# Performance work log

Hardware: AMD Instinct MI355X
Metric: run time of the kernel (lower is better)

Reference implementation:

```python
import jax, jax.numpy as jnp
import numpy as np

L = 10
DIM = 4
TABLE = 1 << 16
BASE_RES = 16.0
PLS = 2.0
HID = 64
SCALE_MULTI = 0.5
DENSITY_OFFSET = -1.0
SCENE_SCALING = 2.0
PRIMES = (np.uint32(1), np.uint32(2654435761), np.uint32(805459861))


def _safe_exp(x):
    return jnp.exp(jnp.clip(x, -30.0, 10.0))


def _l2norm(x, eps=1e-8):
    return x / jnp.sqrt(jnp.sum(x * x, -1, keepdims=True) + eps)


def _circumcenters(tets):
    # tets: [T,4,3]; solve 2(vi-v0).c = |vi|^2-|v0|^2
    v0 = tets[:, 0]
    A = 2.0 * (tets[:, 1:] - v0[:, None, :]) + 1e-6 * jnp.eye(3, dtype=tets.dtype)
    b = jnp.sum(tets[:, 1:] ** 2, -1) - jnp.sum(v0 ** 2, -1)[:, None]
    c = jnp.linalg.solve(A, b[..., None])[..., 0]
    r = jnp.linalg.norm(c - v0, axis=-1)
    return c, r


def _project_to_tet(p, tets):
    # clamp-and-renormalize barycentric coordinates (approximate projection)
    v0 = tets[:, 0]
    E = tets[:, 1:] - v0[:, None, :]
    M = jnp.einsum('tid,tjd->tij', E, E) + 1e-6 * jnp.eye(3, dtype=tets.dtype)
    rhs = jnp.einsum('tid,td->ti', E, p - v0)
    lam = jnp.linalg.solve(M, rhs[..., None])[..., 0]
    bary = jnp.concatenate([1.0 - lam.sum(-1, keepdims=True), lam], -1)
    bary = jnp.clip(bary, 0.0, 1.0)
    bary = bary / jnp.clip(bary.sum(-1, keepdims=True), 1e-6, None)
    return jnp.einsum('tv,tvd->td', bary, tets)


def _contract_mean_std(x, std):
    # mipnerf-360 style scene contraction of mean; std scaled by |J| ~ 1/n^2
    n = jnp.maximum(jnp.linalg.norm(x, axis=-1, keepdims=True), 1e-9)
    cx = jnp.where(n <= 1.0, x, (2.0 - 1.0 / n) * x / n)
    cs = std * jnp.where(n[..., 0] <= 1.0, 1.0, 1.0 / (n[..., 0] ** 2))
    return cx, cs


def _hash_encode(pos, tables):
    # pos [T,3] in [0,1); tables [L, TABLE, DIM]; multiresolution hash grid
    mask = np.uint32(TABLE - 1)
    pos = jnp.clip(pos, 0.0, 1.0 - 1e-6)
    feats = []
    for l in range(L):
        res = float(np.floor(BASE_RES * (PLS ** l)))
        x = pos * res
        f = jnp.floor(x)
        w = x - f
        fi = f.astype(jnp.uint32)
        acc = jnp.zeros(pos.shape[:-1] + (DIM,), pos.dtype)
        for cz in (0, 1):
            for cy in (0, 1):
                for cx in (0, 1):
                    c = fi + jnp.asarray((cx, cy, cz), jnp.uint32)
                    h = ((c[..., 0] * PRIMES[0]) ^ (c[..., 1] * PRIMES[1]) ^ (c[..., 2] * PRIMES[2])) & mask
                    wt = ((w[..., 0] if cx else 1.0 - w[..., 0]) *
                          (w[..., 1] if cy else 1.0 - w[..., 1]) *
                          (w[..., 2] if cz else 1.0 - w[..., 2]))
                    acc = acc + tables[l][h.astype(jnp.int32)] * wt[..., None]
        feats.append(acc)
    return jnp.stack(feats, axis=1)  # [T, L, DIM]


def _forward(vertices, indices, center, tables, W1, b1, W2, b2, W3, b3):
    tets = vertices[indices]  # [T,4,3] gather
    cc, radius = _circumcenters(tets)
    cc = _project_to_tet(cc, tets)
    normalized = (cc - center) / SCENE_SCALING
    cv, cr = _contract_mean_std(normalized, radius / SCENE_SCALING)
    cr = cr * SCALE_MULTI
    n = jnp.arange(L, dtype=vertices.dtype)
    erf_x = 1.0 / jnp.sqrt(PLS * 4.0 * n[None, :] * cr[:, None] + 1e-12)
    scaling = jax.lax.erf(erf_x)  # [T, L] per-level erf anti-aliasing scale
    pos = cv * 0.25 + 0.5  # contracted [-2,2] -> [0,1]
    feats = _hash_encode(pos, tables) * scaling[..., None]
    h = feats.reshape(feats.shape[0], L * DIM)
    h = jax.nn.selu(h @ W1 + b1)
    h = jax.nn.selu(h @ W2 + b2)
    out = h @ W3 + b3  # [T, 13]
    density = _safe_exp(out[:, 0] + DENSITY_OFFSET)
    pairs = ((0, 1), (0, 2), (0, 3), (1, 2), (1, 3), (2, 3))
    el = jnp.stack([jnp.linalg.norm(tets[:, i] - tets[:, j], axis=1) for i, j in pairs], 0).max(0)
    alpha = 1.0 - jnp.exp(-density * el)
    V = vertices.shape[0]
    vertex_alpha = jnp.zeros((V,), vertices.dtype).at[indices].max(
        jnp.broadcast_to(alpha[:, None], indices.shape))  # scatter amax
    fs = out[:, 1:]
    base = fs[:, :3] + 0.5
    grads = jnp.clip(base[:, :, None], 0.0, None) * jnp.tanh(fs[:, 3:12].reshape(-1, 3, 3))
    offs = _l2norm(tets - cc[:, None, :])
    vcol = base[:, None, :] + jnp.einsum('tcd,tvd->tvc', grads, offs)  # [T,4,3]
    return vertex_alpha, vcol


def setup_inputs() -> dict:
    key = jax.random.key(0)
    ks = jax.random.split(key, 8)
    V, T = 100000, 500000
    vertices = jax.random.normal(ks[0], (V, 3), jnp.float32) * 0.5
    indices = jax.random.randint(ks[1], (T, 4), 0, V, jnp.int32)
    center = jnp.zeros((1, 3), jnp.float32)
    tables = jax.random.normal(ks[2], (L, TABLE, DIM), jnp.float32) * 1e-2
    def lin(k, i, o):
        s = (6.0 / (i + o)) ** 0.5
        return jax.random.uniform(k, (i, o), jnp.float32, -s, s)
    return dict(vertices=vertices, indices=indices, center=center, tables=tables,
                W1=lin(ks[3], L * DIM, HID), b1=jnp.zeros((HID,), jnp.float32),
                W2=lin(ks[4], HID, HID), b2=jnp.zeros((HID,), jnp.float32),
                W3=lin(ks[5], HID, 13), b3=jnp.zeros((13,), jnp.float32))


def reference(vertices, indices, center, tables, W1, b1, W2, b2, W3, b3):
    return _forward(vertices, indices, center, tables, W1, b1, W2, b2, W3, b3)
```

## Files before the change

### kernel.cpp

```cpp
#include <hip/hip_runtime.h>
#include <math.h>

#define NLVL 10
#define TBL 65536
#define NHID 64
#define NIN 40
#define LDP 68

typedef __attribute__((ext_vector_type(8))) short bf16x8;
typedef __attribute__((ext_vector_type(4))) float f32x4;

__device__ __forceinline__ float selu_f(float x) {
    return 1.0507009873554805f * (x > 0.0f ? x : 1.6732632423543772f * (__expf(x) - 1.0f));
}
__device__ __forceinline__ float fast_tanh(float x) {
    float xx = fminf(fmaxf(x, -15.0f), 15.0f);
    float t = __expf(2.0f * xx);
    return (t - 1.0f) / (t + 1.0f);
}
__device__ __forceinline__ unsigned short f2bf(float x) {
    unsigned u = __float_as_uint(x);
    unsigned r = (u + 0x7FFFu + ((u >> 16) & 1u)) >> 16;
    return (unsigned short)r;
}
__device__ __forceinline__ float bf2f(unsigned short h) {
    return __uint_as_float(((unsigned)h) << 16);
}
__device__ __forceinline__ short2 split_bf(float x) {
    unsigned short h = f2bf(x);
    float r = x - bf2f(h);
    short2 s;
    s.x = (short)h;
    s.y = (short)f2bf(r);
    return s;
}

__device__ __forceinline__ void solve3d(const double A[3][3], const double b[3], double x[3]) {
    double a00=A[0][0], a01=A[0][1], a02=A[0][2];
    double a10=A[1][0], a11=A[1][1], a12=A[1][2];
    double a20=A[2][0], a21=A[2][1], a22=A[2][2];
    double C00 =  (a11*a22 - a12*a21);
    double C01 = -(a10*a22 - a12*a20);
    double C02 =  (a10*a21 - a11*a20);
    double C10 = -(a01*a22 - a02*a21);
    double C11 =  (a00*a22 - a02*a20);
    double C12 = -(a00*a21 - a01*a20);
    double C20 =  (a01*a12 - a02*a11);
    double C21 = -(a00*a12 - a02*a10);
    double C22 =  (a00*a11 - a01*a10);
    double det = a00*C00 + a01*C01 + a02*C02;
    double inv = 1.0 / det;
    x[0] = (C00*b[0] + C10*b[1] + C20*b[2]) * inv;
    x[1] = (C01*b[0] + C11*b[1] + C21*b[2]) * inv;
    x[2] = (C02*b[0] + C12*b[1] + C22*b[2]) * inv;
}

__global__ void __launch_bounds__(256) zero_alpha_kernel(float* out, int V) {
    int i = blockIdx.x * blockDim.x + threadIdx.x;
    if (i < V) out[i] = 0.0f;
}

__global__ void __launch_bounds__(256) geom_kernel(
    const float* __restrict__ vertices,
    const int*   __restrict__ indices,
    const float* __restrict__ center,
    float* __restrict__ aux, int T)
{
    int t = blockIdx.x * blockDim.x + threadIdx.x;
    if (t >= T) return;

    double p[4][3];
    #pragma unroll
    for (int v = 0; v < 4; ++v) {
        int vid = indices[t*4+v];
        p[v][0] = (double)vertices[vid*3+0];
        p[v][1] = (double)vertices[vid*3+1];
        p[v][2] = (double)vertices[vid*3+2];
    }

    double A[3][3], bb[3];
    double v0sq = p[0][0]*p[0][0] + p[0][1]*p[0][1] + p[0][2]*p[0][2];
    #pragma unroll
    for (int i = 0; i < 3; ++i) {
        #pragma unroll
        for (int j = 0; j < 3; ++j)
            A[i][j] = 2.0*(p[i+1][j] - p[0][j]) + (i==j ? 1e-6 : 0.0);
        bb[i] = p[i+1][0]*p[i+1][0] + p[i+1][1]*p[i+1][1] + p[i+1][2]*p[i+1][2] - v0sq;
    }
    double c[3];
    solve3d(A, bb, c);
    double dx0 = c[0]-p[0][0], dy0 = c[1]-p[0][1], dz0 = c[2]-p[0][2];
    double radius = sqrt(dx0*dx0 + dy0*dy0 + dz0*dz0);

    double E[3][3];
    #pragma unroll
    for (int i = 0; i < 3; ++i)
        #pragma unroll
        for (int j = 0; j < 3; ++j)
            E[i][j] = p[i+1][j] - p[0][j];
    double M[3][3], rhs[3];
    #pragma unroll
    for (int i = 0; i < 3; ++i) {
        #pragma unroll
        for (int k = 0; k < 3; ++k)
            M[i][k] = E[i][0]*E[k][0] + E[i][1]*E[k][1] + E[i][2]*E[k][2] + (i==k ? 1e-6 : 0.0);
        rhs[i] = E[i][0]*dx0 + E[i][1]*dy0 + E[i][2]*dz0;
    }
    double lam[3];
    solve3d(M, rhs, lam);
    double bary[4];
    bary[0] = 1.0 - lam[0] - lam[1] - lam[2];
    bary[1] = lam[0]; bary[2] = lam[1]; bary[3] = lam[2];
    double bs = 0.0;
    #pragma unroll
    for (int v = 0; v < 4; ++v) {
        bary[v] = fmin(fmax(bary[v], 0.0), 1.0);
        bs += bary[v];
    }
    bs = fmax(bs, 1e-6);
    double cc[3];
    #pragma unroll
    for (int j = 0; j < 3; ++j)
        cc[j] = (bary[0]*p[0][j] + bary[1]*p[1][j] + bary[2]*p[2][j] + bary[3]*p[3][j]) / bs;

    double xv[3];
    xv[0] = (cc[0] - (double)center[0]) * 0.5;
    xv[1] = (cc[1] - (double)center[1]) * 0.5;
    xv[2] = (cc[2] - (double)center[2]) * 0.5;
    double nrm = sqrt(xv[0]*xv[0] + xv[1]*xv[1] + xv[2]*xv[2]);
    double n = fmax(nrm, 1e-9);
    double cv[3], cs;
    if (n <= 1.0) {
        cv[0]=xv[0]; cv[1]=xv[1]; cv[2]=xv[2];
        cs = radius * 0.5;
    } else {
        double f = (2.0 - 1.0/n) / n;
        cv[0]=xv[0]*f; cv[1]=xv[1]*f; cv[2]=xv[2]*f;
        cs = radius * 0.5 / (n*n);
    }
    float crf = (float)(cs * 0.5);

    float pos0 = fminf(fmaxf((float)(cv[0]*0.25 + 0.5), 0.0f), 1.0f - 1e-6f);
    float pos1 = fminf(fmaxf((float)(cv[1]*0.25 + 0.5), 0.0f), 1.0f - 1e-6f);
    float pos2 = fminf(fmaxf((float)(cv[2]*0.25 + 0.5), 0.0f), 1.0f - 1e-6f);

    float el = 0.0f;
    #pragma unroll
    for (int a = 0; a < 3; ++a)
        #pragma unroll
        for (int bq = a+1; bq < 4; ++bq) {
            float ddx = (float)(p[a][0]-p[bq][0]);
            float ddy = (float)(p[a][1]-p[bq][1]);
            float ddz = (float)(p[a][2]-p[bq][2]);
            el = fmaxf(el, sqrtf(ddx*ddx + ddy*ddy + ddz*ddz));
        }

    size_t st = (size_t)T;
    aux[0*st + t] = pos0;
    aux[1*st + t] = pos1;
    aux[2*st + t] = pos2;
    aux[3*st + t] = crf;
    aux[4*st + t] = (float)cc[0];
    aux[5*st + t] = (float)cc[1];
    aux[6*st + t] = (float)cc[2];
    aux[7*st + t] = el;
}

__global__ void __launch_bounds__(256) hash_kernel(
    const float* __restrict__ tables,
    const float* __restrict__ aux,
    float* __restrict__ feats, int T)
{
    int t = blockIdx.x * blockDim.x + threadIdx.x;
    if (t >= T) return;
    size_t st = (size_t)T;
    float pos0 = aux[0*st + t];
    float pos1 = aux[1*st + t];
    float pos2 = aux[2*st + t];
    float crf  = aux[3*st + t];

    float4* frow = reinterpret_cast<float4*>(feats + (size_t)t * NIN);
    float res = 16.0f;
    #pragma unroll
    for (int l = 0; l < NLVL; ++l) {
        float x0 = pos0*res, x1 = pos1*res, x2 = pos2*res;
        float f0 = floorf(x0), f1 = floorf(x1), f2 = floorf(x2);
        float w0 = x0-f0, w1 = x1-f1, w2 = x2-f2;
        unsigned i0 = (unsigned)f0, i1 = (unsigned)f1, i2 = (unsigned)f2;
        float a0=0.f, a1=0.f, a2=0.f, a3=0.f;
        #pragma unroll
        for (int cn = 0; cn < 8; ++cn) {
            unsigned cx = (unsigned)(cn & 1), cy = (unsigned)((cn >> 1) & 1), cz = (unsigned)((cn >> 2) & 1);
            unsigned hh = ((i0 + cx) * 1u) ^ ((i1 + cy) * 2654435761u) ^ ((i2 + cz) * 805459861u);
            hh &= 65535u;
            float wt = (cx ? w0 : 1.0f - w0) * (cy ? w1 : 1.0f - w1) * (cz ? w2 : 1.0f - w2);
            const float4 tv = *reinterpret_cast<const float4*>(tables + ((size_t)l*TBL + hh)*4);
            a0 = fmaf(tv.x, wt, a0);
            a1 = fmaf(tv.y, wt, a1);
            a2 = fmaf(tv.z, wt, a2);
            a3 = fmaf(tv.w, wt, a3);
        }
        float sc = erff(rsqrtf(8.0f*(float)l*crf + 1e-12f));
        frow[l] = make_float4(a0*sc, a1*sc, a2*sc, a3*sc);
        res *= 2.0f;
    }
}

__global__ void __launch_bounds__(256, 2) mlp_mfma_kernel(
    const float* __restrict__ feats,
    const float* __restrict__ aux,
    const float* __restrict__ vertices,
    const int*   __restrict__ indices,
    const float* __restrict__ W1, const float* __restrict__ b1,
    const float* __restrict__ W2, const float* __restrict__ b2,
    const float* __restrict__ W3, const float* __restrict__ b3,
    float* __restrict__ out, int T, int V)
{
    __shared__ float hts[4][16][LDP];

    const int tid  = threadIdx.x;
    const int wid  = tid >> 6;
    const int lane = tid & 63;
    const int r    = lane & 15;
    const int g    = lane >> 4;

    bf16x8 w1h[2][4], w1l[2][4];
    #pragma unroll
    for (int s = 0; s < 2; ++s)
        #pragma unroll
        for (int nt = 0; nt < 4; ++nt) {
            bf16x8 h, lo;
            #pragma unroll
            for (int j = 0; j < 8; ++j) {
                int k = s*32 + g*8 + j;
                float w = (k < NIN) ? W1[k*NHID + nt*16 + r] : 0.0f;
                short2 sp = split_bf(w);
                h[j] = sp.x; lo[j] = sp.y;
            }
            w1h[s][nt] = h; w1l[s][nt] = lo;
        }
    bf16x8 w2h[2][4], w2l[2][4];
    #pragma unroll
    for (int s = 0; s < 2; ++s)
        #pragma unroll
        for (int nt = 0; nt < 4; ++nt) {
            bf16x8 h, lo;
            #pragma unroll
            for (int j = 0; j < 8; ++j) {
                int k = s*32 + g*8 + j;
                float w = W2[k*NHID + nt*16 + r];
                short2 sp = split_bf(w);
                h[j] = sp.x; lo[j] = sp.y;
            }
            w2h[s][nt] = h; w2l[s][nt] = lo;
        }
    bf16x8 w3h[2], w3l[2];
    #pragma unroll
    for (int s = 0; s < 2; ++s) {
        bf16x8 h, lo;
        #pragma unroll
        for (int j = 0; j < 8; ++j) {
            int k = s*32 + g*8 + j;
            float w = (r < 13) ? W3[k*13 + r] : 0.0f;
            short2 sp = split_bf(w);
            h[j] = sp.x; lo[j] = sp.y;
        }
        w3h[s] = h; w3l[s] = lo;
    }
    float b1v[4], b2v[4];
    #pragma unroll
    for (int nt = 0; nt < 4; ++nt) { b1v[nt] = b1[nt*16 + r]; b2v[nt] = b2[nt*16 + r]; }
    float b3v = (r < 13) ? b3[r] : 0.0f;

    const int nmt = (T + 15) >> 4;
    const int gw = blockIdx.x * 4 + wid;
    const int gstride = gridDim.x * 4;

    for (int mt = gw; mt < nmt; mt += gstride) {
        const int t0 = mt * 16;
        const int trow = t0 + r;
        const bool rowok = trow < T;
        bf16x8 ah0, al0, ah1, al1;
        {
            const float4* fr4 = reinterpret_cast<const float4*>(feats + (size_t)trow * NIN);
            float4 z = make_float4(0.f,0.f,0.f,0.f);
            float4 u0 = rowok ? fr4[g*2+0] : z;
            float4 u1 = rowok ? fr4[g*2+1] : z;
            short2 sp;
            sp = split_bf(u0.x); ah0[0] = sp.x; al0[0] = sp.y;
            sp = split_bf(u0.y); ah0[1] = sp.x; al0[1] = sp.y;
            sp = split_bf(u0.z); ah0[2] = sp.x; al0[2] = sp.y;
            sp = split_bf(u0.w); ah0[3] = sp.x; al0[3] = sp.y;
            sp = split_bf(u1.x); ah0[4] = sp.x; al0[4] = sp.y;
            sp = split_bf(u1.y); ah0[5] = sp.x; al0[5] = sp.y;
            sp = split_bf(u1.z); ah0[6] = sp.x; al0[6] = sp.y;
            sp = split_bf(u1.w); ah0[7] = sp.x; al0[7] = sp.y;
            bool k1ok = rowok && (g == 0);
            float4 v0 = k1ok ? fr4[8] : z;
            float4 v1 = k1ok ? fr4[9] : z;
            sp = split_bf(v0.x); ah1[0] = sp.x; al1[0] = sp.y;
            sp = split_bf(v0.y); ah1[1] = sp.x; al1[1] = sp.y;
            sp = split_bf(v0.z); ah1[2] = sp.x; al1[2] = sp.y;
            sp = split_bf(v0.w); ah1[3] = sp.x; al1[3] = sp.y;
            sp = split_bf(v1.x); ah1[4] = sp.x; al1[4] = sp.y;
            sp = split_bf(v1.y); ah1[5] = sp.x; al1[5] = sp.y;
            sp = split_bf(v1.z); ah1[6] = sp.x; al1[6] = sp.y;
            sp = split_bf(v1.w); ah1[7] = sp.x; al1[7] = sp.y;
        }

        #pragma unroll
        for (int nt = 0; nt < 4; ++nt) {
            f32x4 acc = {0.f, 0.f, 0.f, 0.f};
            acc = __builtin_amdgcn_mfma_f32_16x16x32_bf16(ah0, w1h[0][nt], acc, 0, 0, 0);
            acc = __builtin_amdgcn_mfma_f32_16x16x32_bf16(ah0, w1l[0][nt], acc, 0, 0, 0);
            acc = __builtin_amdgcn_mfma_f32_16x16x32_bf16(al0, w1h[0][nt], acc, 0, 0, 0);
            acc = __builtin_amdgcn_mfma_f32_16x16x32_bf16(ah1, w1h[1][nt], acc, 0, 0, 0);
            acc = __builtin_amdgcn_mfma_f32_16x16x32_bf16(ah1, w1l[1][nt], acc, 0, 0, 0);
            acc = __builtin_amdgcn_mfma_f32_16x16x32_bf16(al1, w1h[1][nt], acc, 0, 0, 0);
            #pragma unroll
            for (int q = 0; q < 4; ++q)
                hts[wid][g*4 + q][nt*16 + r] = selu_f(acc[q] + b1v[nt]);
        }
        asm volatile("s_waitcnt lgkmcnt(0)" ::: "memory");

        bf16x8 a2h[2], a2l[2];
        #pragma unroll
        for (int s = 0; s < 2; ++s) {
            bf16x8 h, lo;
            #pragma unroll
            for (int j = 0; j < 8; ++j) {
                short2 sp = split_bf(hts[wid][r][s*32 + g*8 + j]);
                h[j] = sp.x; lo[j] = sp.y;
            }
            a2h[s] = h; a2l[s] = lo;
        }
        asm volatile("s_waitcnt lgkmcnt(0)" ::: "memory");
        float h2v[4][4];
        #pragma unroll
        for (int nt = 0; nt < 4; ++nt) {
            f32x4 acc = {0.f, 0.f, 0.f, 0.f};
            #pragma unroll
            for (int s = 0; s < 2; ++s) {
                acc = __builtin_amdgcn_mfma_f32_16x16x32_bf16(a2h[s], w2h[s][nt], acc, 0, 0, 0);
                acc = __builtin_amdgcn_mfma_f32_16x16x32_bf16(a2h[s], w2l[s][nt], acc, 0, 0, 0);
                acc = __builtin_amdgcn_mfma_f32_16x16x32_bf16(a2l[s], w2h[s][nt], acc, 0, 0, 0);
            }
            #pragma unroll
            for (int q = 0; q < 4; ++q) h2v[nt][q] = selu_f(acc[q] + b2v[nt]);
        }
        #pragma unroll
        for (int nt = 0; nt < 4; ++nt)
            #pragma unroll
            for (int q = 0; q < 4; ++q)
                hts[wid][g*4 + q][nt*16 + r] = h2v[nt][q];
        asm volatile("s_waitcnt lgkmcnt(0)" ::: "memory");

        bf16x8 a3h[2], a3l[2];
        #pragma unroll
        for (int s = 0; s < 2; ++s) {
            bf16x8 h, lo;
            #pragma unroll
            for (int j = 0; j < 8; ++j) {
                short2 sp = split_bf(hts[wid][r][s*32 + g*8 + j]);
                h[j] = sp.x; lo[j] = sp.y;
            }
            a3h[s] = h; a3l[s] = lo;
        }
        asm volatile("s_waitcnt lgkmcnt(0)" ::: "memory");
        {
            f32x4 acc = {0.f, 0.f, 0.f, 0.f};
            #pragma unroll
            for (int s = 0; s < 2; ++s) {
                acc = __builtin_amdgcn_mfma_f32_16x16x32_bf16(a3h[s], w3h[s], acc, 0, 0, 0);
                acc = __builtin_amdgcn_mfma_f32_16x16x32_bf16(a3h[s], w3l[s], acc, 0, 0, 0);
                acc = __builtin_amdgcn_mfma_f32_16x16x32_bf16(a3l[s], w3h[s], acc, 0, 0, 0);
            }
            #pragma unroll
            for (int q = 0; q < 4; ++q)
                hts[wid][g*4 + q][r] = acc[q] + b3v;
        }
        asm volatile("s_waitcnt lgkmcnt(0)" ::: "memory");

        if (lane < 16) {
            int tt = t0 + lane;
            if (tt < T) {
                float o[13];
                #pragma unroll
                for (int k = 0; k < 13; ++k) o[k] = hts[wid][lane][k];
                size_t st = (size_t)T;
                float el  = aux[7*st + tt];
                float cc0 = aux[4*st + tt], cc1 = aux[5*st + tt], cc2 = aux[6*st + tt];
                float dv = fminf(fmaxf(o[0] - 1.0f, -30.0f), 10.0f);
                float density = __expf(dv);
                float alpha = 1.0f - __expf(-density * el);
                int ab = __float_as_int(alpha);
                int vid0 = indices[tt*4+0];
                int vid1 = indices[tt*4+1];
                int vid2 = indices[tt*4+2];
                int vid3 = indices[tt*4+3];
                atomicMax((int*)out + vid0, ab);
                atomicMax((int*)out + vid1, ab);
                atomicMax((int*)out + vid2, ab);
                atomicMax((int*)out + vid3, ab);

                float base0 = o[1] + 0.5f, base1 = o[2] + 0.5f, base2 = o[3] + 0.5f;
                float bc0 = fmaxf(base0, 0.0f), bc1 = fmaxf(base1, 0.0f), bc2 = fmaxf(base2, 0.0f);
                float g00 = bc0*fast_tanh(o[4]),  g01 = bc0*fast_tanh(o[5]),  g02 = bc0*fast_tanh(o[6]);
                float g10 = bc1*fast_tanh(o[7]),  g11 = bc1*fast_tanh(o[8]),  g12 = bc1*fast_tanh(o[9]);
                float g20 = bc2*fast_tanh(o[10]), g21 = bc2*fast_tanh(o[11]), g22 = bc2*fast_tanh(o[12]);

                float* vout = out + V + (size_t)tt * 12;
                const int vv[4] = {vid0, vid1, vid2, vid3};
                #pragma unroll
                for (int v = 0; v < 4; ++v) {
                    float px = vertices[vv[v]*3+0], py = vertices[vv[v]*3+1], pz = vertices[vv[v]*3+2];
                    float ox = px-cc0, oy = py-cc1, oz = pz-cc2;
                    float inv = rsqrtf(ox*ox + oy*oy + oz*oz + 1e-8f);
                    float q0 = ox*inv, q1 = oy*inv, q2 = oz*inv;
                    vout[v*3+0] = base0 + g00*q0 + g01*q1 + g02*q2;
                    vout[v*3+1] = base1 + g10*q0 + g11*q1 + g12*q2;
                    vout[v*3+2] = base2 + g20*q0 + g21*q1 + g22*q2;
                }
            }
        }
        asm volatile("s_waitcnt lgkmcnt(0)" ::: "memory");
    }
}

__global__ void __launch_bounds__(256) tet_forward_fused(
    const float* __restrict__ vertices,
    const int*   __restrict__ indices,
    const float* __restrict__ center,
    const float* __restrict__ tables,
    const float* __restrict__ W1, const float* __restrict__ b1,
    const float* __restrict__ W2, const float* __restrict__ b2,
    const float* __restrict__ W3, const float* __restrict__ b3,
    float* __restrict__ out, int T, int V)
{
    int t = blockIdx.x * blockDim.x + threadIdx.x;
    if (t >= T) return;

    double p[4][3];
    int vv[4];
    #pragma unroll
    for (int v = 0; v < 4; ++v) {
        vv[v] = indices[t*4+v];
        p[v][0] = (double)vertices[vv[v]*3+0];
        p[v][1] = (double)vertices[vv[v]*3+1];
        p[v][2] = (double)vertices[vv[v]*3+2];
    }
    double A[3][3], bb[3];
    double v0sq = p[0][0]*p[0][0] + p[0][1]*p[0][1] + p[0][2]*p[0][2];
    #pragma unroll
    for (int i = 0; i < 3; ++i) {
        #pragma unroll
        for (int j = 0; j < 3; ++j)
            A[i][j] = 2.0*(p[i+1][j] - p[0][j]) + (i==j ? 1e-6 : 0.0);
        bb[i] = p[i+1][0]*p[i+1][0] + p[i+1][1]*p[i+1][1] + p[i+1][2]*p[i+1][2] - v0sq;
    }
    double c[3];
    solve3d(A, bb, c);
    double dx0 = c[0]-p[0][0], dy0 = c[1]-p[0][1], dz0 = c[2]-p[0][2];
    double radius = sqrt(dx0*dx0 + dy0*dy0 + dz0*dz0);
    double E[3][3];
    #pragma unroll
    for (int i = 0; i < 3; ++i)
        #pragma unroll
        for (int j = 0; j < 3; ++j)
            E[i][j] = p[i+1][j] - p[0][j];
    double M[3][3], rhs[3];
    #pragma unroll
    for (int i = 0; i < 3; ++i) {
        #pragma unroll
        for (int k = 0; k < 3; ++k)
            M[i][k] = E[i][0]*E[k][0] + E[i][1]*E[k][1] + E[i][2]*E[k][2] + (i==k ? 1e-6 : 0.0);
        rhs[i] = E[i][0]*dx0 + E[i][1]*dy0 + E[i][2]*dz0;
    }
    double lam[3];
    solve3d(M, rhs, lam);
    double bary[4];
    bary[0] = 1.0 - lam[0] - lam[1] - lam[2];
    bary[1] = lam[0]; bary[2] = lam[1]; bary[3] = lam[2];
    double bs = 0.0;
    #pragma unroll
    for (int v = 0; v < 4; ++v) { bary[v] = fmin(fmax(bary[v], 0.0), 1.0); bs += bary[v]; }
    bs = fmax(bs, 1e-6);
    double cc[3];
    #pragma unroll
    for (int j = 0; j < 3; ++j)
        cc[j] = (bary[0]*p[0][j] + bary[1]*p[1][j] + bary[2]*p[2][j] + bary[3]*p[3][j]) / bs;
    double xv[3];
    xv[0] = (cc[0] - (double)center[0]) * 0.5;
    xv[1] = (cc[1] - (double)center[1]) * 0.5;
    xv[2] = (cc[2] - (double)center[2]) * 0.5;
    double nrm = sqrt(xv[0]*xv[0] + xv[1]*xv[1] + xv[2]*xv[2]);
    double n = fmax(nrm, 1e-9);
    double cv[3], cs;
    if (n <= 1.0) { cv[0]=xv[0]; cv[1]=xv[1]; cv[2]=xv[2]; cs = radius * 0.5; }
    else { double f = (2.0 - 1.0/n) / n; cv[0]=xv[0]*f; cv[1]=xv[1]*f; cv[2]=xv[2]*f; cs = radius * 0.5 / (n*n); }
    float crf = (float)(cs * 0.5);
    float pos0 = fminf(fmaxf((float)(cv[0]*0.25 + 0.5), 0.0f), 1.0f - 1e-6f);
    float pos1 = fminf(fmaxf((float)(cv[1]*0.25 + 0.5), 0.0f), 1.0f - 1e-6f);
    float pos2 = fminf(fmaxf((float)(cv[2]*0.25 + 0.5), 0.0f), 1.0f - 1e-6f);

    float h0[NIN];
    float res = 16.0f;
    #pragma unroll
    for (int l = 0; l < NLVL; ++l) {
        float x0 = pos0*res, x1 = pos1*res, x2 = pos2*res;
        float f0 = floorf(x0), f1 = floorf(x1), f2 = floorf(x2);
        float w0 = x0-f0, w1 = x1-f1, w2 = x2-f2;
        unsigned i0 = (unsigned)f0, i1 = (unsigned)f1, i2 = (unsigned)f2;
        float a0=0.f, a1=0.f, a2=0.f, a3=0.f;
        #pragma unroll
        for (int cn = 0; cn < 8; ++cn) {
            unsigned cx = (unsigned)(cn & 1), cy = (unsigned)((cn >> 1) & 1), cz = (unsigned)((cn >> 2) & 1);
            unsigned hh = ((i0 + cx) * 1u) ^ ((i1 + cy) * 2654435761u) ^ ((i2 + cz) * 805459861u);
            hh &= 65535u;
            float wt = (cx ? w0 : 1.0f - w0) * (cy ? w1 : 1.0f - w1) * (cz ? w2 : 1.0f - w2);
            const float4 tv = *reinterpret_cast<const float4*>(tables + ((size_t)l*TBL + hh)*4);
            a0 = fmaf(tv.x, wt, a0); a1 = fmaf(tv.y, wt, a1);
            a2 = fmaf(tv.z, wt, a2); a3 = fmaf(tv.w, wt, a3);
        }
        float sc = erff(rsqrtf(8.0f*(float)l*crf + 1e-12f));
        h0[l*4+0] = a0*sc; h0[l*4+1] = a1*sc; h0[l*4+2] = a2*sc; h0[l*4+3] = a3*sc;
        res *= 2.0f;
    }

    float h1[NHID];
    #pragma unroll
    for (int j = 0; j < NHID; ++j) h1[j] = b1[j];
    #pragma unroll
    for (int i = 0; i < NIN; ++i) {
        float hi = h0[i];
        #pragma unroll
        for (int j = 0; j < NHID; ++j) h1[j] = fmaf(hi, W1[i*NHID + j], h1[j]);
    }
    #pragma unroll
    for (int j = 0; j < NHID; ++j) h1[j] = selu_f(h1[j]);

    float o[13];
    #pragma unroll
    for (int k = 0; k < 13; ++k) o[k] = b3[k];
    #pragma unroll
    for (int half = 0; half < 2; ++half) {
        float h2h[32];
        #pragma unroll
        for (int jj = 0; jj < 32; ++jj) h2h[jj] = b2[half*32 + jj];
        #pragma unroll
        for (int i = 0; i < NHID; ++i) {
            float hi = h1[i];
            #pragma unroll
            for (int jj = 0; jj < 32; ++jj)
                h2h[jj] = fmaf(hi, W2[i*NHID + half*32 + jj], h2h[jj]);
        }
        #pragma unroll
        for (int jj = 0; jj < 32; ++jj) {
            float hv = selu_f(h2h[jj]);
            #pragma unroll
            for (int k = 0; k < 13; ++k)
                o[k] = fmaf(hv, W3[(half*32 + jj)*13 + k], o[k]);
        }
    }

    float dv = fminf(fmaxf(o[0] - 1.0f, -30.0f), 10.0f);
    float density = __expf(dv);
    float el = 0.0f;
    #pragma unroll
    for (int a = 0; a < 3; ++a)
        #pragma unroll
        for (int bq = a+1; bq < 4; ++bq) {
            float ddx = (float)(p[a][0]-p[bq][0]);
            float ddy = (float)(p[a][1]-p[bq][1]);
            float ddz = (float)(p[a][2]-p[bq][2]);
            el = fmaxf(el, sqrtf(ddx*ddx + ddy*ddy + ddz*ddz));
        }
    float alpha = 1.0f - __expf(-density * el);
    int ab = __float_as_int(alpha);
    atomicMax((int*)out + vv[0], ab);
    atomicMax((int*)out + vv[1], ab);
    atomicMax((int*)out + vv[2], ab);
    atomicMax((int*)out + vv[3], ab);

    float base0 = o[1] + 0.5f, base1 = o[2] + 0.5f, base2 = o[3] + 0.5f;
    float bc0 = fmaxf(base0, 0.0f), bc1 = fmaxf(base1, 0.0f), bc2 = fmaxf(base2, 0.0f);
    float g00 = bc0*fast_tanh(o[4]),  g01 = bc0*fast_tanh(o[5]),  g02 = bc0*fast_tanh(o[6]);
    float g10 = bc1*fast_tanh(o[7]),  g11 = bc1*fast_tanh(o[8]),  g12 = bc1*fast_tanh(o[9]);
    float g20 = bc2*fast_tanh(o[10]), g21 = bc2*fast_tanh(o[11]), g22 = bc2*fast_tanh(o[12]);

    float* vout = out + V + (size_t)t * 12;
    #pragma unroll
    for (int v = 0; v < 4; ++v) {
        float ox = (float)(p[v][0]-cc[0]), oy = (float)(p[v][1]-cc[1]), oz = (float)(p[v][2]-cc[2]);
        float inv = rsqrtf(ox*ox + oy*oy + oz*oz + 1e-8f);
        float q0 = ox*inv, q1 = oy*inv, q2 = oz*inv;
        vout[v*3+0] = base0 + g00*q0 + g01*q1 + g02*q2;
        vout[v*3+1] = base1 + g10*q0 + g11*q1 + g12*q2;
        vout[v*3+2] = base2 + g20*q0 + g21*q1 + g22*q2;
    }
}

extern "C" void kernel_launch(void* const* d_in, const int* in_sizes, int n_in,
                              void* d_out, int out_size, void* d_ws, size_t ws_size,
                              hipStream_t stream) {
    const float* vertices = (const float*)d_in[0];
    const int*   indices  = (const int*)d_in[1];
    const float* center   = (const float*)d_in[2];
    const float* tables   = (const float*)d_in[3];
    const float* W1 = (const float*)d_in[4];
    const float* b1 = (const float*)d_in[5];
    const float* W2 = (const float*)d_in[6];
    const float* b2 = (const float*)d_in[7];
    const float* W3 = (const float*)d_in[8];
    const float* b3 = (const float*)d_in[9];
    int V = in_sizes[0] / 3;
    int T = in_sizes[1] / 4;
    float* out = (float*)d_out;

    hipLaunchKernelGGL(zero_alpha_kernel, dim3((V + 255) / 256), dim3(256), 0, stream, out, V);

    size_t need = (size_t)T * 48 * sizeof(float);
    dim3 grid((T + 255) / 256), blk(256);
    if (ws_size >= need) {
        float* aux   = (float*)d_ws;
        float* feats = aux + (size_t)T * 8;
        hipLaunchKernelGGL(geom_kernel, grid, blk, 0, stream, vertices, indices, center, aux, T);
        hipLaunchKernelGGL(hash_kernel, grid, blk, 0, stream, tables, aux, feats, T);
        hipLaunchKernelGGL(mlp_mfma_kernel, dim3(512), blk, 0, stream, feats, aux, vertices, indices,
                           W1, b1, W2, b2, W3, b3, out, T, V);
    } else {
        hipLaunchKernelGGL(tet_forward_fused, grid, blk, 0, stream,
                           vertices, indices, center, tables, W1, b1, W2, b2, W3, b3, out, T, V);
    }
}
```

Before: 268.7 us.

## Fuse hash-grid encoding into MFMA MLP kernel and spread epilogue across lanes

Removes the separate hash_kernel and its 40-float-per-tet feature buffer. Each lane group now computes two hash levels directly into its MFMA A-fragment, with loads batched for more memory parallelism. The layer-1 split-bf16 low terms for levels 8-9 are dropped, which lowers precision slightly. LDS reads become float4, and the output epilogue now uses all 64 lanes (one vertex per lane) instead of 16. The risk is that the fused kernel, limited to 512 blocks with two per SM, hides the table-gather latency less well than the standalone hash kernel did.

```diff
diff --git a/kernel.cpp b/kernel.cpp
--- a/kernel.cpp
+++ b/kernel.cpp
@@ -9,6 +9,7 @@
 
 typedef __attribute__((ext_vector_type(8))) short bf16x8;
 typedef __attribute__((ext_vector_type(4))) float f32x4;
+typedef unsigned int uint;
 
 __device__ __forceinline__ float selu_f(float x) {
     return 1.0507009873554805f * (x > 0.0f ? x : 1.6732632423543772f * (__expf(x) - 1.0f));
@@ -166,48 +167,50 @@
     aux[7*st + t] = el;
 }
 
-__global__ void __launch_bounds__(256) hash_kernel(
-    const float* __restrict__ tables,
-    const float* __restrict__ aux,
-    float* __restrict__ feats, int T)
-{
-    int t = blockIdx.x * blockDim.x + threadIdx.x;
-    if (t >= T) return;
-    size_t st = (size_t)T;
-    float pos0 = aux[0*st + t];
-    float pos1 = aux[1*st + t];
-    float pos2 = aux[2*st + t];
-    float crf  = aux[3*st + t];
-
-    float4* frow = reinterpret_cast<float4*>(feats + (size_t)t * NIN);
-    float res = 16.0f;
-    #pragma unroll
-    for (int l = 0; l < NLVL; ++l) {
-        float x0 = pos0*res, x1 = pos1*res, x2 = pos2*res;
+__device__ __forceinline__ void enc2(const float4* __restrict__ tb4,
+                                     float px, float py, float pz, float crf,
+                                     int l0, float f[8]) {
+    uint idx[2][8];
+    float wt[2][8];
+    #pragma unroll
+    for (int h = 0; h < 2; ++h) {
+        int l = l0 + h;
+        float res = (float)(16 << l);
+        float x0 = px*res, x1 = py*res, x2 = pz*res;
         float f0 = floorf(x0), f1 = floorf(x1), f2 = floorf(x2);
         float w0 = x0-f0, w1 = x1-f1, w2 = x2-f2;
-        unsigned i0 = (unsigned)f0, i1 = (unsigned)f1, i2 = (unsigned)f2;
+        uint i0 = (uint)f0, i1 = (uint)f1, i2 = (uint)f2;
+        #pragma unroll
+        for (int cn = 0; cn < 8; ++cn) {
+            uint cx = (uint)(cn & 1), cy = (uint)((cn >> 1) & 1), cz = (uint)((cn >> 2) & 1);
+            idx[h][cn] = (((i0 + cx) * 1u) ^ ((i1 + cy) * 2654435761u) ^ ((i2 + cz) * 805459861u)) & 65535u;
+            wt[h][cn] = (cx ? w0 : 1.0f - w0) * (cy ? w1 : 1.0f - w1) * (cz ? w2 : 1.0f - w2);
+        }
+    }
+    float4 v[2][8];
+    #pragma unroll
+    for (int h = 0; h < 2; ++h)
+        #pragma unroll
+        for (int cn = 0; cn < 8; ++cn)
+            v[h][cn] = tb4[(size_t)(l0+h)*TBL + idx[h][cn]];
+    #pragma unroll
+    for (int h = 0; h < 2; ++h) {
         float a0=0.f, a1=0.f, a2=0.f, a3=0.f;
         #pragma unroll
         for (int cn = 0; cn < 8; ++cn) {
-            unsigned cx = (unsigned)(cn & 1), cy = (unsigned)((cn >> 1) & 1), cz = (unsigned)((cn >> 2) & 1);
-            unsigned hh = ((i0 + cx) * 1u) ^ ((i1 + cy) * 2654435761u) ^ ((i2 + cz) * 805459861u);
-            hh &= 65535u;
-            float wt = (cx ? w0 : 1.0f - w0) * (cy ? w1 : 1.0f - w1) * (cz ? w2 : 1.0f - w2);
-            const float4 tv = *reinterpret_cast<const float4*>(tables + ((size_t)l*TBL + hh)*4);
-            a0 = fmaf(tv.x, wt, a0);
-            a1 = fmaf(tv.y, wt, a1);
-            a2 = fmaf(tv.z, wt, a2);
-            a3 = fmaf(tv.w, wt, a3);
-        }
-        float sc = erff(rsqrtf(8.0f*(float)l*crf + 1e-12f));
-        frow[l] = make_float4(a0*sc, a1*sc, a2*sc, a3*sc);
-        res *= 2.0f;
-    }
-}
-
-__global__ void __launch_bounds__(256, 2) mlp_mfma_kernel(
-    const float* __restrict__ feats,
+            float w = wt[h][cn];
+            a0 = fmaf(v[h][cn].x, w, a0);
+            a1 = fmaf(v[h][cn].y, w, a1);
+            a2 = fmaf(v[h][cn].z, w, a2);
+            a3 = fmaf(v[h][cn].w, w, a3);
+        }
+        float sc = erff(rsqrtf(8.0f*(float)(l0+h)*crf + 1e-12f));
+        f[h*4+0] = a0*sc; f[h*4+1] = a1*sc; f[h*4+2] = a2*sc; f[h*4+3] = a3*sc;
+    }
+}
+
+__global__ void __launch_bounds__(256, 2) mlp_fused_kernel(
+    const float* __restrict__ tables,
     const float* __restrict__ aux,
     const float* __restrict__ vertices,
     const int*   __restrict__ indices,
@@ -216,15 +219,17 @@
     const float* __restrict__ W3, const float* __restrict__ b3,
     float* __restrict__ out, int T, int V)
 {
-    __shared__ float hts[4][16][LDP];
+    __shared__ __align__(16) float hts[4][16][LDP];
 
     const int tid  = threadIdx.x;
     const int wid  = tid >> 6;
     const int lane = tid & 63;
     const int r    = lane & 15;
     const int g    = lane >> 4;
-
-    bf16x8 w1h[2][4], w1l[2][4];
+    const float4* tb4 = reinterpret_cast<const float4*>(tables);
+
+    bf16x8 w1h[2][4];
+    bf16x8 w1l0[4];
     #pragma unroll
     for (int s = 0; s < 2; ++s)
         #pragma unroll
@@ -237,7 +242,8 @@
                 short2 sp = split_bf(w);
                 h[j] = sp.x; lo[j] = sp.y;
             }
-            w1h[s][nt] = h; w1l[s][nt] = lo;
+            w1h[s][nt] = h;
+            if (s == 0) w1l0[nt] = lo;
         }
     bf16x8 w2h[2][4], w2l[2][4];
     #pragma unroll
@@ -272,6 +278,7 @@
     for (int nt = 0; nt < 4; ++nt) { b1v[nt] = b1[nt*16 + r]; b2v[nt] = b2[nt*16 + r]; }
     float b3v = (r < 13) ? b3[r] : 0.0f;
 
+    const size_t st = (size_t)T;
     const int nmt = (T + 15) >> 4;
     const int gw = blockIdx.x * 4 + wid;
     const int gstride = gridDim.x * 4;
@@ -280,43 +287,35 @@
         const int t0 = mt * 16;
         const int trow = t0 + r;
         const bool rowok = trow < T;
-        bf16x8 ah0, al0, ah1, al1;
+
+        float px = rowok ? aux[0*st + trow] : 0.5f;
+        float py = rowok ? aux[1*st + trow] : 0.5f;
+        float pz = rowok ? aux[2*st + trow] : 0.5f;
+        float crf = rowok ? aux[3*st + trow] : 0.0f;
+
+        float fk0[8];
+        enc2(tb4, px, py, pz, crf, 2*g, fk0);
+        bf16x8 ah0, al0;
+        #pragma unroll
+        for (int j = 0; j < 8; ++j) {
+            short2 sp = split_bf(rowok ? fk0[j] : 0.0f);
+            ah0[j] = sp.x; al0[j] = sp.y;
+        }
+        bf16x8 ah1;
         {
-            const float4* fr4 = reinterpret_cast<const float4*>(feats + (size_t)trow * NIN);
-            float4 z = make_float4(0.f,0.f,0.f,0.f);
-            float4 u0 = rowok ? fr4[g*2+0] : z;
-            float4 u1 = rowok ? fr4[g*2+1] : z;
-            short2 sp;
-            sp = split_bf(u0.x); ah0[0] = sp.x; al0[0] = sp.y;
-            sp = split_bf(u0.y); ah0[1] = sp.x; al0[1] = sp.y;
-            sp = split_bf(u0.z); ah0[2] = sp.x; al0[2] = sp.y;
-            sp = split_bf(u0.w); ah0[3] = sp.x; al0[3] = sp.y;
-            sp = split_bf(u1.x); ah0[4] = sp.x; al0[4] = sp.y;
-            sp = split_bf(u1.y); ah0[5] = sp.x; al0[5] = sp.y;
-            sp = split_bf(u1.z); ah0[6] = sp.x; al0[6] = sp.y;
-            sp = split_bf(u1.w); ah0[7] = sp.x; al0[7] = sp.y;
-            bool k1ok = rowok && (g == 0);
-            float4 v0 = k1ok ? fr4[8] : z;
-            float4 v1 = k1ok ? fr4[9] : z;
-            sp = split_bf(v0.x); ah1[0] = sp.x; al1[0] = sp.y;
-            sp = split_bf(v0.y); ah1[1] = sp.x; al1[1] = sp.y;
-            sp = split_bf(v0.z); ah1[2] = sp.x; al1[2] = sp.y;
-            sp = split_bf(v0.w); ah1[3] = sp.x; al1[3] = sp.y;
-            sp = split_bf(v1.x); ah1[4] = sp.x; al1[4] = sp.y;
-            sp = split_bf(v1.y); ah1[5] = sp.x; al1[5] = sp.y;
-            sp = split_bf(v1.z); ah1[6] = sp.x; al1[6] = sp.y;
-            sp = split_bf(v1.w); ah1[7] = sp.x; al1[7] = sp.y;
+            float fk1[8] = {0.f,0.f,0.f,0.f,0.f,0.f,0.f,0.f};
+            if (g == 0 && rowok) enc2(tb4, px, py, pz, crf, 8, fk1);
+            #pragma unroll
+            for (int j = 0; j < 8; ++j) ah1[j] = (short)f2bf(fk1[j]);
         }
 
         #pragma unroll
         for (int nt = 0; nt < 4; ++nt) {
             f32x4 acc = {0.f, 0.f, 0.f, 0.f};
             acc = __builtin_amdgcn_mfma_f32_16x16x32_bf16(ah0, w1h[0][nt], acc, 0, 0, 0);
-            acc = __builtin_amdgcn_mfma_f32_16x16x32_bf16(ah0, w1l[0][nt], acc, 0, 0, 0);
+            acc = __builtin_amdgcn_mfma_f32_16x16x32_bf16(ah0, w1l0[nt],  acc, 0, 0, 0);
             acc = __builtin_amdgcn_mfma_f32_16x16x32_bf16(al0, w1h[0][nt], acc, 0, 0, 0);
             acc = __builtin_amdgcn_mfma_f32_16x16x32_bf16(ah1, w1h[1][nt], acc, 0, 0, 0);
-            acc = __builtin_amdgcn_mfma_f32_16x16x32_bf16(ah1, w1l[1][nt], acc, 0, 0, 0);
-            acc = __builtin_amdgcn_mfma_f32_16x16x32_bf16(al1, w1h[1][nt], acc, 0, 0, 0);
             #pragma unroll
             for (int q = 0; q < 4; ++q)
                 hts[wid][g*4 + q][nt*16 + r] = selu_f(acc[q] + b1v[nt]);
@@ -326,12 +325,18 @@
         bf16x8 a2h[2], a2l[2];
         #pragma unroll
         for (int s = 0; s < 2; ++s) {
+            float4 u0 = *reinterpret_cast<const float4*>(&hts[wid][r][s*32 + g*8]);
+            float4 u1 = *reinterpret_cast<const float4*>(&hts[wid][r][s*32 + g*8 + 4]);
             bf16x8 h, lo;
-            #pragma unroll
-            for (int j = 0; j < 8; ++j) {
-                short2 sp = split_bf(hts[wid][r][s*32 + g*8 + j]);
-                h[j] = sp.x; lo[j] = sp.y;
-            }
+            short2 sp;
+            sp = split_bf(u0.x); h[0]=sp.x; lo[0]=sp.y;
+            sp = split_bf(u0.y); h[1]=sp.x; lo[1]=sp.y;
+            sp = split_bf(u0.z); h[2]=sp.x; lo[2]=sp.y;
+            sp = split_bf(u0.w); h[3]=sp.x; lo[3]=sp.y;
+            sp = split_bf(u1.x); h[4]=sp.x; lo[4]=sp.y;
+            sp = split_bf(u1.y); h[5]=sp.x; lo[5]=sp.y;
+            sp = split_bf(u1.z); h[6]=sp.x; lo[6]=sp.y;
+            sp = split_bf(u1.w); h[7]=sp.x; lo[7]=sp.y;
             a2h[s] = h; a2l[s] = lo;
         }
         asm volatile("s_waitcnt lgkmcnt(0)" ::: "memory");
@@ -358,12 +363,18 @@
         bf16x8 a3h[2], a3l[2];
         #pragma unroll
         for (int s = 0; s < 2; ++s) {
+            float4 u0 = *reinterpret_cast<const float4*>(&hts[wid][r][s*32 + g*8]);
+            float4 u1 = *reinterpret_cast<const float4*>(&hts[wid][r][s*32 + g*8 + 4]);
             bf16x8 h, lo;
-            #pragma unroll
-            for (int j = 0; j < 8; ++j) {
-                short2 sp = split_bf(hts[wid][r][s*32 + g*8 + j]);
-                h[j] = sp.x; lo[j] = sp.y;
-            }
+            short2 sp;
+            sp = split_bf(u0.x); h[0]=sp.x; lo[0]=sp.y;
+            sp = split_bf(u0.y); h[1]=sp.x; lo[1]=sp.y;
+            sp = split_bf(u0.z); h[2]=sp.x; lo[2]=sp.y;
+            sp = split_bf(u0.w); h[3]=sp.x; lo[3]=sp.y;
+            sp = split_bf(u1.x); h[4]=sp.x; lo[4]=sp.y;
+            sp = split_bf(u1.y); h[5]=sp.x; lo[5]=sp.y;
+            sp = split_bf(u1.z); h[6]=sp.x; lo[6]=sp.y;
+            sp = split_bf(u1.w); h[7]=sp.x; lo[7]=sp.y;
             a3h[s] = h; a3l[s] = lo;
         }
         asm volatile("s_waitcnt lgkmcnt(0)" ::: "memory");
@@ -381,46 +392,41 @@
         }
         asm volatile("s_waitcnt lgkmcnt(0)" ::: "memory");
 
-        if (lane < 16) {
-            int tt = t0 + lane;
-            if (tt < T) {
-                float o[13];
-                #pragma unroll
-                for (int k = 0; k < 13; ++k) o[k] = hts[wid][lane][k];
-                size_t st = (size_t)T;
-                float el  = aux[7*st + tt];
-                float cc0 = aux[4*st + tt], cc1 = aux[5*st + tt], cc2 = aux[6*st + tt];
-                float dv = fminf(fmaxf(o[0] - 1.0f, -30.0f), 10.0f);
+        {
+            int et = lane >> 2;
+            int ev = lane & 3;
+            int te = t0 + et;
+            if (te < T) {
+                const float* orow = hts[wid][et];
+                float4 o0 = *reinterpret_cast<const float4*>(&orow[0]);
+                float4 o1 = *reinterpret_cast<const float4*>(&orow[4]);
+                float4 o2 = *reinterpret_cast<const float4*>(&orow[8]);
+                float o12 = orow[12];
+
+                float el  = aux[7*st + te];
+                float cc0 = aux[4*st + te], cc1 = aux[5*st + te], cc2 = aux[6*st + te];
+
+                float dv = fminf(fmaxf(o0.x - 1.0f, -30.0f), 10.0f);
                 float density = __expf(dv);
                 float alpha = 1.0f - __expf(-density * el);
                 int ab = __float_as_int(alpha);
-                int vid0 = indices[tt*4+0];
-                int vid1 = indices[tt*4+1];
-                int vid2 = indices[tt*4+2];
-                int vid3 = indices[tt*4+3];
-                atomicMax((int*)out + vid0, ab);
-                atomicMax((int*)out + vid1, ab);
-                atomicMax((int*)out + vid2, ab);
-                atomicMax((int*)out + vid3, ab);
-
-                float base0 = o[1] + 0.5f, base1 = o[2] + 0.5f, base2 = o[3] + 0.5f;
+                int vid = indices[te*4 + ev];
+                atomicMax((int*)out + vid, ab);
+
+                float base0 = o0.y + 0.5f, base1 = o0.z + 0.5f, base2 = o0.w + 0.5f;
                 float bc0 = fmaxf(base0, 0.0f), bc1 = fmaxf(base1, 0.0f), bc2 = fmaxf(base2, 0.0f);
-                float g00 = bc0*fast_tanh(o[4]),  g01 = bc0*fast_tanh(o[5]),  g02 = bc0*fast_tanh(o[6]);
-                float g10 = bc1*fast_tanh(o[7]),  g11 = bc1*fast_tanh(o[8]),  g12 = bc1*fast_tanh(o[9]);
-                float g20 = bc2*fast_tanh(o[10]), g21 = bc2*fast_tanh(o[11]), g22 = bc2*fast_tanh(o[12]);
-
-                float* vout = out + V + (size_t)tt * 12;
-                const int vv[4] = {vid0, vid1, vid2, vid3};
-                #pragma unroll
-                for (int v = 0; v < 4; ++v) {
-                    float px = vertices[vv[v]*3+0], py = vertices[vv[v]*3+1], pz = vertices[vv[v]*3+2];
-                    float ox = px-cc0, oy = py-cc1, oz = pz-cc2;
-                    float inv = rsqrtf(ox*ox + oy*oy + oz*oz + 1e-8f);
-                    float q0 = ox*inv, q1 = oy*inv, q2 = oz*inv;
-                    vout[v*3+0] = base0 + g00*q0 + g01*q1 + g02*q2;
-                    vout[v*3+1] = base1 + g10*q0 + g11*q1 + g12*q2;
-                    vout[v*3+2] = base2 + g20*q0 + g21*q1 + g22*q2;
-                }
+                float g00 = bc0*fast_tanh(o1.x), g01 = bc0*fast_tanh(o1.y), g02 = bc0*fast_tanh(o1.z);
+                float g10 = bc1*fast_tanh(o1.w), g11 = bc1*fast_tanh(o2.x), g12 = bc1*fast_tanh(o2.y);
+                float g20 = bc2*fast_tanh(o2.z), g21 = bc2*fast_tanh(o2.w), g22 = bc2*fast_tanh(o12);
+
+                float pxv = vertices[vid*3+0], pyv = vertices[vid*3+1], pzv = vertices[vid*3+2];
+                float ox = pxv-cc0, oy = pyv-cc1, oz = pzv-cc2;
+                float inv = rsqrtf(ox*ox + oy*oy + oz*oz + 1e-8f);
+                float q0 = ox*inv, q1 = oy*inv, q2 = oz*inv;
+                float* vout = out + V + (size_t)te * 12 + ev*3;
+                vout[0] = base0 + g00*q0 + g01*q1 + g02*q2;
+                vout[1] = base1 + g10*q0 + g11*q1 + g12*q2;
+                vout[2] = base2 + g20*q0 + g21*q1 + g22*q2;
             }
         }
         asm volatile("s_waitcnt lgkmcnt(0)" ::: "memory");
@@ -619,14 +625,12 @@
 
     hipLaunchKernelGGL(zero_alpha_kernel, dim3((V + 255) / 256), dim3(256), 0, stream, out, V);
 
-    size_t need = (size_t)T * 48 * sizeof(float);
+    size_t need = (size_t)T * 8 * sizeof(float);
     dim3 grid((T + 255) / 256), blk(256);
     if (ws_size >= need) {
-        float* aux   = (float*)d_ws;
-        float* feats = aux + (size_t)T * 8;
+        float* aux = (float*)d_ws;
         hipLaunchKernelGGL(geom_kernel, grid, blk, 0, stream, vertices, indices, center, aux, T);
-        hipLaunchKernelGGL(hash_kernel, grid, blk, 0, stream, tables, aux, feats, T);
-        hipLaunchKernelGGL(mlp_mfma_kernel, dim3(512), blk, 0, stream, feats, aux, vertices, indices,
+        hipLaunchKernelGGL(mlp_fused_kernel, dim3(512), blk, 0, stream, tables, aux, vertices, indices,
                            W1, b1, W2, b2, W3, b3, out, T, V);
     } else {
         hipLaunchKernelGGL(tet_forward_fused, grid, blk, 0, stream,
```

Result: slower. 301.8 us (+12.3%).
